# Kernel tuning notes

Hardware: AMD Instinct MI355X
Metric: run time of the kernel (lower is better)

The kernel has to match this reference:

```python
import jax, jax.numpy as jnp
import numpy as np

B, Q, S, D, H, F = 16, 8, 4096, 2048, 16, 128  # batch, new tokens, past kv, d_state, heads, head_dim
W_SCALE = 0.02  # keep projections well-conditioned for stable softmax


def setup_inputs() -> dict:
    key = jax.random.key(0)
    ks = jax.random.split(key, 8)
    return {
        "x": jax.random.normal(ks[0], (B, Q, D), jnp.float32),
        "cache_k": jax.random.normal(ks[1], (B, S, H, F), jnp.float32),
        "cache_v": jax.random.normal(ks[2], (B, S, H, F), jnp.float32),
        "wq": jax.random.normal(ks[3], (D, H, F), jnp.float32) * W_SCALE,
        "bq": jnp.zeros((H, F), jnp.float32),
        "wk": jax.random.normal(ks[4], (D, H, F), jnp.float32) * W_SCALE,
        "bk": jnp.zeros((H, F), jnp.float32),
        "wv": jax.random.normal(ks[5], (D, H, F), jnp.float32) * W_SCALE,
        "bv": jnp.zeros((H, F), jnp.float32),
        "wo": jax.random.normal(ks[6], (H, F, D), jnp.float32) * W_SCALE,
        "bo": jnp.zeros((D,), jnp.float32),
    }


def reference(x, cache_k, cache_v, wq, bq, wk, bk, wv, bv, wo, bo):
    # QKV projections: DenseGeneral(features=(H, F), axis=-1)
    q = jnp.einsum("bqd,dhf->bqhf", x, wq) + bq          # [B,Q,H,F]
    k_new = jnp.einsum("bqd,dhf->bqhf", x, wk) + bk      # [B,Q,H,F]
    v_new = jnp.einsum("bqd,dhf->bqhf", x, wv) + bv
    # concat-based KV cache growth along the sequence axis (axis=1)
    k = jnp.concatenate([cache_k, k_new], axis=1)        # [B,S+Q,H,F]
    v = jnp.concatenate([cache_v, v_new], axis=1)
    # full dot-product attention over the whole cache (mask=None on decode path)
    scale = 1.0 / jnp.sqrt(jnp.asarray(F, q.dtype))
    scores = jnp.einsum("bqhf,bkhf->bhqk", q, k) * scale  # [B,H,Q,S+Q]
    probs = jax.nn.softmax(scores, axis=-1)
    attn = jnp.einsum("bhqk,bkhf->bhqf", probs, v)        # [B,H,Q,F]
    # output projection: DenseGeneral(features=D, axis=(-3,-1)) contracts (H, F)
    out = jnp.einsum("bhqf,hfd->bqd", attn, wo) + bo      # [B,Q,D]
    return (out, k, v)
```

## Files before the change

### kernel.cpp

```cpp
#include <hip/hip_runtime.h>
#include <hip/hip_bf16.h>

constexpr int Bc = 16;
constexpr int Qc = 8;
constexpr int Sc = 4096;
constexpr int Dc = 2048;
constexpr int Hc = 16;
constexpr int Fc = 128;
constexpr int SP = Sc + Qc;
constexpr int Mr = Bc * Qc;
constexpr int CHUNK = 256;
constexpr int NCHUNK = 16;
constexpr float SCALE = 0.08838834764831845f;
constexpr float LOG2E = 1.4426950408889634f;
constexpr float QSCALE = SCALE * LOG2E;
constexpr int GKS = 8;
constexpr int GKS_O = 16;

typedef float floatx4 __attribute__((ext_vector_type(4)));

__device__ __forceinline__ float4 nt_load4(const float* p) {
    floatx4 r = __builtin_nontemporal_load(reinterpret_cast<const floatx4*>(p));
    return make_float4(r.x, r.y, r.z, r.w);
}
__device__ __forceinline__ void nt_store4(float* p, float4 v) {
    floatx4 r; r.x = v.x; r.y = v.y; r.z = v.z; r.w = v.w;
    __builtin_nontemporal_store(r, reinterpret_cast<floatx4*>(p));
}

template<int KS>
__global__ __launch_bounds__(256)
void gemm_ksplit(const float* __restrict__ A, const float* __restrict__ W0,
                 const float* __restrict__ W1, const float* __restrict__ W2,
                 float* __restrict__ part)
{
    constexpr int KC = Dc / KS;
    const int ntile = blockIdx.x;
    const int mat   = blockIdx.y;
    const int kz    = blockIdx.z;
    const float* __restrict__ W = (mat == 0) ? W0 : ((mat == 1) ? W1 : W2);
    const int t  = threadIdx.x;
    const int tx = t & 15, ty = t >> 4;
    const int r0 = ty * 8, c0 = tx * 8;
    const int ncol0 = ntile * 128;

    __shared__ float a_s[16][132];
    __shared__ float w_s[16][128];

    float acc[8][8] = {};

    const int kbase = kz * KC;
    for (int k0 = kbase; k0 < kbase + KC; k0 += 16) {
        {
            const int kk = t & 15, r = t >> 4;
            #pragma unroll
            for (int i = 0; i < 8; i++)
                a_s[kk][r + i * 16] = A[(size_t)(r + i * 16) * Dc + k0 + kk];
        }
        {
            const int nn = t & 127, ks_ = t >> 7;
            #pragma unroll
            for (int i = 0; i < 8; i++)
                w_s[ks_ + i * 2][nn] = W[(size_t)(k0 + ks_ + i * 2) * 2048 + ncol0 + nn];
        }
        __syncthreads();
        #pragma unroll
        for (int kk = 0; kk < 16; kk++) {
            const float4 av0 = *reinterpret_cast<const float4*>(&a_s[kk][r0]);
            const float4 av1 = *reinterpret_cast<const float4*>(&a_s[kk][r0 + 4]);
            const float4 wv0 = *reinterpret_cast<const float4*>(&w_s[kk][c0]);
            const float4 wv1 = *reinterpret_cast<const float4*>(&w_s[kk][c0 + 4]);
            const float av[8] = {av0.x, av0.y, av0.z, av0.w, av1.x, av1.y, av1.z, av1.w};
            const float wv[8] = {wv0.x, wv0.y, wv0.z, wv0.w, wv1.x, wv1.y, wv1.z, wv1.w};
            #pragma unroll
            for (int i = 0; i < 8; i++)
                #pragma unroll
                for (int j = 0; j < 8; j++)
                    acc[i][j] += av[i] * wv[j];
        }
        __syncthreads();
    }
    float* __restrict__ dst = part + (size_t)(mat * KS + kz) * Mr * 2048;
    #pragma unroll
    for (int i = 0; i < 8; i++)
        #pragma unroll
        for (int j = 0; j < 8; j++)
            dst[(size_t)(r0 + i) * 2048 + ncol0 + c0 + j] = acc[i][j];
}

__global__ __launch_bounds__(256)
void reduce_qkv(const float* __restrict__ part, const float* __restrict__ bq,
                const float* __restrict__ bk, const float* __restrict__ bv,
                float* __restrict__ q_ws, float* __restrict__ out_k, float* __restrict__ out_v)
{
    const int mat = blockIdx.y;
    const int e4 = blockIdx.x * 256 + threadIdx.x;
    const int e = e4 * 4;
    const int m = e >> 11, n = e & 2047;
    const float* __restrict__ p = part + (size_t)mat * GKS * (Mr * 2048);
    float4 s = make_float4(0, 0, 0, 0);
    #pragma unroll
    for (int ks = 0; ks < GKS; ks++) {
        const float4 a = *reinterpret_cast<const float4*>(&p[(size_t)ks * (Mr * 2048) + e]);
        s.x += a.x; s.y += a.y; s.z += a.z; s.w += a.w;
    }
    const int b = m >> 3, qi = m & 7;
    if (mat == 0) {
        const float4 bb = *reinterpret_cast<const float4*>(&bq[n]);
        s.x += bb.x; s.y += bb.y; s.z += bb.z; s.w += bb.w;
        *reinterpret_cast<float4*>(&q_ws[e]) = s;
    } else if (mat == 1) {
        const float4 bb = *reinterpret_cast<const float4*>(&bk[n]);
        s.x += bb.x; s.y += bb.y; s.z += bb.z; s.w += bb.w;
        *reinterpret_cast<float4*>(&out_k[((size_t)(b * SP + Sc + qi)) * 2048 + n]) = s;
    } else {
        const float4 bb = *reinterpret_cast<const float4*>(&bv[n]);
        s.x += bb.x; s.y += bb.y; s.z += bb.z; s.w += bb.w;
        *reinterpret_cast<float4*>(&out_v[((size_t)(b * SP + Sc + qi)) * 2048 + n]) = s;
    }
}

__global__ __launch_bounds__(1024, 4)
void attn_fused(const float* __restrict__ cache_k, const float* __restrict__ cache_v,
                const float* __restrict__ q_ws,
                float* __restrict__ out_k, float* __restrict__ out_v,
                float* __restrict__ part_acc, float* __restrict__ part_l)
{
    const int c = blockIdx.x;
    const int b = blockIdx.y;
    const int t = threadIdx.x;
    const int lane = t & 63;
    const int hwid = t >> 5;
    const int h = hwid & 15;
    const int par = hwid >> 4;
    const int fl = lane & 31;
    const int s0 = c * CHUNK;

    __shared__ float wacc_s[Hc][Qc][Fc];
    __shared__ float l_s[Hc][Qc];

    const int sel1 = fl & 1, sel2 = (fl >> 1) & 1, sel3 = (fl >> 2) & 1;
    const int myqi = 4 * sel1 + 2 * sel2 + sel3;
    int baddr[Qc];
    #pragma unroll
    for (int qi = 0; qi < Qc; qi++) {
        const int slot = ((qi >> 2) & 1) | (((qi >> 1) & 1) << 1) | ((qi & 1) << 2);
        baddr[qi] = (lane & ~7) | slot;
    }

    float4 qreg[Qc];
    #pragma unroll
    for (int qi = 0; qi < Qc; qi++) {
        float4 qv = *reinterpret_cast<const float4*>(
            &q_ws[((size_t)(b * Qc + qi)) * Dc + h * Fc + fl * 4]);
        qv.x *= QSCALE; qv.y *= QSCALE; qv.z *= QSCALE; qv.w *= QSCALE;
        qreg[qi] = qv;
    }

    float4 acc[Qc];
    float lsum = 0.f;
    #pragma unroll
    for (int i = 0; i < Qc; i++) acc[i] = make_float4(0, 0, 0, 0);

    const int rowoff = h * Fc + fl * 4;

    #pragma unroll 2
    for (int n = 0; n < CHUNK / 2; n++) {
        const int key = s0 + 2 * n + par;
        const size_t coff = ((size_t)(b * Sc + key)) * 2048 + rowoff;
        const size_t ooff = ((size_t)(b * SP + key)) * 2048 + rowoff;
        const float4 kv = nt_load4(&cache_k[coff]);
        const float4 vv = nt_load4(&cache_v[coff]);
        nt_store4(&out_k[ooff], kv);
        nt_store4(&out_v[ooff], vv);

        float p[Qc];
        #pragma unroll
        for (int qi = 0; qi < Qc; qi++)
            p[qi] = kv.x * qreg[qi].x + kv.y * qreg[qi].y
                  + kv.z * qreg[qi].z + kv.w * qreg[qi].w;
        float a1[4];
        #pragma unroll
        for (int i = 0; i < 4; i++) {
            const float send = sel1 ? p[i] : p[i + 4];
            const float keep = sel1 ? p[i + 4] : p[i];
            a1[i] = keep + __shfl_xor(send, 1, 64);
        }
        float a2[2];
        #pragma unroll
        for (int i = 0; i < 2; i++) {
            const float send = sel2 ? a1[i] : a1[i + 2];
            const float keep = sel2 ? a1[i + 2] : a1[i];
            a2[i] = keep + __shfl_xor(send, 2, 64);
        }
        float s_ = (sel3 ? a2[1] : a2[0]) + __shfl_xor(sel3 ? a2[0] : a2[1], 4, 64);
        s_ += __shfl_xor(s_, 8, 64);
        s_ += __shfl_xor(s_, 16, 64);
        const float e = __builtin_amdgcn_exp2f(s_);
        lsum += e;
        #pragma unroll
        for (int qi = 0; qi < Qc; qi++) {
            const float pe = __shfl(e, baddr[qi], 64);
            acc[qi].x += pe * vv.x; acc[qi].y += pe * vv.y;
            acc[qi].z += pe * vv.z; acc[qi].w += pe * vv.w;
        }
    }

    if (c == NCHUNK - 1) {
        #pragma unroll
        for (int m = 0; m < Qc / 2; m++) {
            const int key = Sc + 2 * m + par;
            const size_t ooff = ((size_t)(b * SP + key)) * 2048 + rowoff;
            const float4 kv = *reinterpret_cast<const float4*>(&out_k[ooff]);
            const float4 vv = *reinterpret_cast<const float4*>(&out_v[ooff]);

            float p[Qc];
            #pragma unroll
            for (int qi = 0; qi < Qc; qi++)
                p[qi] = kv.x * qreg[qi].x + kv.y * qreg[qi].y
                      + kv.z * qreg[qi].z + kv.w * qreg[qi].w;
            float a1[4];
            #pragma unroll
            for (int i = 0; i < 4; i++) {
                const float send = sel1 ? p[i] : p[i + 4];
                const float keep = sel1 ? p[i + 4] : p[i];
                a1[i] = keep + __shfl_xor(send, 1, 64);
            }
            float a2[2];
            #pragma unroll
            for (int i = 0; i < 2; i++) {
                const float send = sel2 ? a1[i] : a1[i + 2];
                const float keep = sel2 ? a1[i + 2] : a1[i];
                a2[i] = keep + __shfl_xor(send, 2, 64);
            }
            float s_ = (sel3 ? a2[1] : a2[0]) + __shfl_xor(sel3 ? a2[0] : a2[1], 4, 64);
            s_ += __shfl_xor(s_, 8, 64);
            s_ += __shfl_xor(s_, 16, 64);
            const float e = __builtin_amdgcn_exp2f(s_);
            lsum += e;
            #pragma unroll
            for (int qi = 0; qi < Qc; qi++) {
                const float pe = __shfl(e, baddr[qi], 64);
                acc[qi].x += pe * vv.x; acc[qi].y += pe * vv.y;
                acc[qi].z += pe * vv.z; acc[qi].w += pe * vv.w;
            }
        }
    }

    if (par == 0) {
        #pragma unroll
        for (int qi = 0; qi < Qc; qi++)
            *reinterpret_cast<float4*>(&wacc_s[h][qi][fl * 4]) = acc[qi];
        if (fl < 8) l_s[h][myqi] = lsum;
    }
    __syncthreads();
    if (par == 1) {
        const size_t idx = (size_t)(b * Hc + h) * NCHUNK + c;
        #pragma unroll
        for (int qi = 0; qi < Qc; qi++) {
            const float4 a = *reinterpret_cast<const float4*>(&wacc_s[h][qi][fl * 4]);
            float4 s_;
            s_.x = a.x + acc[qi].x; s_.y = a.y + acc[qi].y;
            s_.z = a.z + acc[qi].z; s_.w = a.w + acc[qi].w;
            *reinterpret_cast<float4*>(&part_acc[(idx * Qc + qi) * Fc + fl * 4]) = s_;
        }
        if (fl < 8) part_l[idx * Qc + myqi] = l_s[h][myqi] + lsum;
    }
}

__global__ __launch_bounds__(256)
void attn_combine(const float* __restrict__ part_acc, const float* __restrict__ part_l,
                  float* __restrict__ attn_ws)
{
    const int bh = blockIdx.x;
    const int b = bh >> 4, h = bh & 15;
    const int t = threadIdx.x;
    const int qi = t >> 5, f4 = (t & 31) * 4;
    const size_t base = (size_t)bh * NCHUNK;

    float lg = 0.f;
    #pragma unroll
    for (int c = 0; c < NCHUNK; c++) lg += part_l[(base + c) * Qc + qi];
    float4 s_ = make_float4(0, 0, 0, 0);
    #pragma unroll
    for (int c = 0; c < NCHUNK; c++) {
        const float4 a = *reinterpret_cast<const float4*>(
            &part_acc[((base + c) * Qc + qi) * Fc + f4]);
        s_.x += a.x; s_.y += a.y; s_.z += a.z; s_.w += a.w;
    }
    const float inv = 1.0f / lg;
    const float4 o = make_float4(s_.x * inv, s_.y * inv, s_.z * inv, s_.w * inv);
    *reinterpret_cast<float4*>(&attn_ws[((size_t)(b * Qc + qi)) * Dc + h * Fc + f4]) = o;
}

__global__ __launch_bounds__(256)
void reduce_o(const float* __restrict__ part, const float* __restrict__ bo,
              float* __restrict__ out)
{
    const int e4 = blockIdx.x * 256 + threadIdx.x;
    const int e = e4 * 4;
    const int n = e & 2047;
    float4 s = make_float4(0, 0, 0, 0);
    #pragma unroll
    for (int ks = 0; ks < GKS_O; ks++) {
        const float4 a = *reinterpret_cast<const float4*>(&part[(size_t)ks * (Mr * 2048) + e]);
        s.x += a.x; s.y += a.y; s.z += a.z; s.w += a.w;
    }
    const float4 bb = *reinterpret_cast<const float4*>(&bo[n]);
    s.x += bb.x; s.y += bb.y; s.z += bb.z; s.w += bb.w;
    *reinterpret_cast<float4*>(&out[e]) = s;
}

extern "C" void kernel_launch(void* const* d_in, const int* in_sizes, int n_in,
                              void* d_out, int out_size, void* d_ws, size_t ws_size,
                              hipStream_t stream)
{
    (void)in_sizes; (void)n_in; (void)out_size; (void)ws_size;
    const float* x       = (const float*)d_in[0];
    const float* cache_k = (const float*)d_in[1];
    const float* cache_v = (const float*)d_in[2];
    const float* wq      = (const float*)d_in[3];
    const float* bq      = (const float*)d_in[4];
    const float* wk      = (const float*)d_in[5];
    const float* bk      = (const float*)d_in[6];
    const float* wv      = (const float*)d_in[7];
    const float* bv      = (const float*)d_in[8];
    const float* wo      = (const float*)d_in[9];
    const float* bo      = (const float*)d_in[10];

    float* out   = (float*)d_out;
    float* out_k = out + (size_t)Mr * Dc;
    float* out_v = out_k + (size_t)Bc * SP * Hc * Fc;

    float* ws       = (float*)d_ws;
    float* q_ws     = ws;
    float* attn_ws  = ws + 262144;
    float* part_l   = ws + 524288;
    float* gemm_part = ws + 557056;
    float* part_acc = gemm_part;

    gemm_ksplit<GKS><<<dim3(16, 3, GKS), 256, 0, stream>>>(x, wq, wk, wv, gemm_part);
    reduce_qkv<<<dim3(256, 3), 256, 0, stream>>>(gemm_part, bq, bk, bv, q_ws, out_k, out_v);
    attn_fused<<<dim3(NCHUNK, Bc), 1024, 0, stream>>>(
        cache_k, cache_v, q_ws, out_k, out_v, part_acc, part_l);
    attn_combine<<<dim3(Bc * Hc), 256, 0, stream>>>(part_acc, part_l, attn_ws);
    gemm_ksplit<GKS_O><<<dim3(16, 1, GKS_O), 256, 0, stream>>>(attn_ws, wo, wo, wo, gemm_part);
    reduce_o<<<dim3(256), 256, 0, stream>>>(gemm_part, bo, out);
}
```

Before: 505.4 us.

## Split attention chunk into score pass and PV pass via shared memory

The single key loop is split into two passes. The first loads K, computes exp scores and writes them to a shared-memory buffer of CHUNK×H×Q floats. The second loads V and reads those scores back as float4s, replacing eight cross-lane shuffles per key with two LDS loads. Shared memory grows to about 128KB per block, which may limit occupancy. Each thread only reads scores its own wave wrote, since lanes with fl<8 of the same wave store them.

```diff
diff --git a/kernel.cpp b/kernel.cpp
--- a/kernel.cpp
+++ b/kernel.cpp
@@ -136,7 +136,7 @@
     const int fl = lane & 31;
     const int s0 = c * CHUNK;
 
-    __shared__ float wacc_s[Hc][Qc][Fc];
+    __shared__ float sc_s[CHUNK][Hc][Qc];
     __shared__ float l_s[Hc][Qc];
 
     const int sel1 = fl & 1, sel2 = (fl >> 1) & 1, sel3 = (fl >> 2) & 1;
@@ -166,13 +166,12 @@
 
     #pragma unroll 2
     for (int n = 0; n < CHUNK / 2; n++) {
-        const int key = s0 + 2 * n + par;
+        const int kl = 2 * n + par;
+        const int key = s0 + kl;
         const size_t coff = ((size_t)(b * Sc + key)) * 2048 + rowoff;
         const size_t ooff = ((size_t)(b * SP + key)) * 2048 + rowoff;
         const float4 kv = nt_load4(&cache_k[coff]);
-        const float4 vv = nt_load4(&cache_v[coff]);
         nt_store4(&out_k[ooff], kv);
-        nt_store4(&out_v[ooff], vv);
 
         float p[Qc];
         #pragma unroll
@@ -198,12 +197,28 @@
         s_ += __shfl_xor(s_, 16, 64);
         const float e = __builtin_amdgcn_exp2f(s_);
         lsum += e;
-        #pragma unroll
-        for (int qi = 0; qi < Qc; qi++) {
-            const float pe = __shfl(e, baddr[qi], 64);
-            acc[qi].x += pe * vv.x; acc[qi].y += pe * vv.y;
-            acc[qi].z += pe * vv.z; acc[qi].w += pe * vv.w;
-        }
+        if (fl < 8) sc_s[kl][h][myqi] = e;
+    }
+
+    #pragma unroll 2
+    for (int n = 0; n < CHUNK / 2; n++) {
+        const int kl = 2 * n + par;
+        const int key = s0 + kl;
+        const size_t coff = ((size_t)(b * Sc + key)) * 2048 + rowoff;
+        const size_t ooff = ((size_t)(b * SP + key)) * 2048 + rowoff;
+        const float4 vv = nt_load4(&cache_v[coff]);
+        nt_store4(&out_v[ooff], vv);
+
+        const float4 e0 = *reinterpret_cast<const float4*>(&sc_s[kl][h][0]);
+        const float4 e1 = *reinterpret_cast<const float4*>(&sc_s[kl][h][4]);
+        acc[0].x += e0.x * vv.x; acc[0].y += e0.x * vv.y; acc[0].z += e0.x * vv.z; acc[0].w += e0.x * vv.w;
+        acc[1].x += e0.y * vv.x; acc[1].y += e0.y * vv.y; acc[1].z += e0.y * vv.z; acc[1].w += e0.y * vv.w;
+        acc[2].x += e0.z * vv.x; acc[2].y += e0.z * vv.y; acc[2].z += e0.z * vv.z; acc[2].w += e0.z * vv.w;
+        acc[3].x += e0.w * vv.x; acc[3].y += e0.w * vv.y; acc[3].z += e0.w * vv.z; acc[3].w += e0.w * vv.w;
+        acc[4].x += e1.x * vv.x; acc[4].y += e1.x * vv.y; acc[4].z += e1.x * vv.z; acc[4].w += e1.x * vv.w;
+        acc[5].x += e1.y * vv.x; acc[5].y += e1.y * vv.y; acc[5].z += e1.y * vv.z; acc[5].w += e1.y * vv.w;
+        acc[6].x += e1.z * vv.x; acc[6].y += e1.z * vv.y; acc[6].z += e1.z * vv.z; acc[6].w += e1.z * vv.w;
+        acc[7].x += e1.w * vv.x; acc[7].y += e1.w * vv.y; acc[7].z += e1.w * vv.z; acc[7].w += e1.w * vv.w;
     }
 
     if (c == NCHUNK - 1) {
@@ -247,10 +262,12 @@
         }
     }
 
+    __syncthreads();
+    float* wacc = &sc_s[0][0][0];
     if (par == 0) {
         #pragma unroll
         for (int qi = 0; qi < Qc; qi++)
-            *reinterpret_cast<float4*>(&wacc_s[h][qi][fl * 4]) = acc[qi];
+            *reinterpret_cast<float4*>(&wacc[(h * Qc + qi) * Fc + fl * 4]) = acc[qi];
         if (fl < 8) l_s[h][myqi] = lsum;
     }
     __syncthreads();
@@ -258,7 +275,7 @@
         const size_t idx = (size_t)(b * Hc + h) * NCHUNK + c;
         #pragma unroll
         for (int qi = 0; qi < Qc; qi++) {
-            const float4 a = *reinterpret_cast<const float4*>(&wacc_s[h][qi][fl * 4]);
+            const float4 a = *reinterpret_cast<const float4*>(&wacc[(h * Qc + qi) * Fc + fl * 4]);
             float4 s_;
             s_.x = a.x + acc[qi].x; s_.y = a.y + acc[qi].y;
             s_.z = a.z + acc[qi].z; s_.w = a.w + acc[qi].w;
```

New measurement: 514.8 us. No clear change (+1.9%).

## Fuse split-K and attention reductions into producers via last-block atomic counters

Applied to the files above, without the earlier changes.

Removes the three separate reduction kernels (reduce_qkv, attn_combine, reduce_o) by having the last-arriving block of each group, detected with an atomic counter after a threadfence, perform the reduction and bias add inside the producing kernel. This cuts kernel launches and inter-kernel gaps but adds a memset for the counters. The reduction work is now done by only a few blocks per group, so it runs with less parallelism than the standalone kernels had.

```diff
diff --git a/kernel.cpp b/kernel.cpp
--- a/kernel.cpp
+++ b/kernel.cpp
@@ -28,13 +28,16 @@
     __builtin_nontemporal_store(r, reinterpret_cast<floatx4*>(p));
 }
 
-template<int KS>
 __global__ __launch_bounds__(256)
-void gemm_ksplit(const float* __restrict__ A, const float* __restrict__ W0,
-                 const float* __restrict__ W1, const float* __restrict__ W2,
-                 float* __restrict__ part)
+void gemm_qkv(const float* __restrict__ A, const float* __restrict__ W0,
+              const float* __restrict__ W1, const float* __restrict__ W2,
+              const float* __restrict__ bq, const float* __restrict__ bk,
+              const float* __restrict__ bv,
+              float* __restrict__ part, float* __restrict__ q_ws,
+              float* __restrict__ out_k, float* __restrict__ out_v,
+              int* __restrict__ cnt)
 {
-    constexpr int KC = Dc / KS;
+    constexpr int KC = Dc / GKS;
     const int ntile = blockIdx.x;
     const int mat   = blockIdx.y;
     const int kz    = blockIdx.z;
@@ -46,19 +49,18 @@
 
     __shared__ float a_s[16][132];
     __shared__ float w_s[16][128];
+    __shared__ int is_last;
 
     float acc[8][8] = {};
 
     const int kbase = kz * KC;
     for (int k0 = kbase; k0 < kbase + KC; k0 += 16) {
-        {
-            const int kk = t & 15, r = t >> 4;
+        {   const int kk = t & 15, r = t >> 4;
             #pragma unroll
             for (int i = 0; i < 8; i++)
                 a_s[kk][r + i * 16] = A[(size_t)(r + i * 16) * Dc + k0 + kk];
         }
-        {
-            const int nn = t & 127, ks_ = t >> 7;
+        {   const int nn = t & 127, ks_ = t >> 7;
             #pragma unroll
             for (int i = 0; i < 8; i++)
                 w_s[ks_ + i * 2][nn] = W[(size_t)(k0 + ks_ + i * 2) * 2048 + ncol0 + nn];
@@ -80,43 +82,42 @@
         }
         __syncthreads();
     }
-    float* __restrict__ dst = part + (size_t)(mat * KS + kz) * Mr * 2048;
+    float* __restrict__ dst = part + (size_t)(mat * GKS + kz) * Mr * 2048;
     #pragma unroll
     for (int i = 0; i < 8; i++)
         #pragma unroll
         for (int j = 0; j < 8; j++)
             dst[(size_t)(r0 + i) * 2048 + ncol0 + c0 + j] = acc[i][j];
-}
-
-__global__ __launch_bounds__(256)
-void reduce_qkv(const float* __restrict__ part, const float* __restrict__ bq,
-                const float* __restrict__ bk, const float* __restrict__ bv,
-                float* __restrict__ q_ws, float* __restrict__ out_k, float* __restrict__ out_v)
-{
-    const int mat = blockIdx.y;
-    const int e4 = blockIdx.x * 256 + threadIdx.x;
-    const int e = e4 * 4;
-    const int m = e >> 11, n = e & 2047;
-    const float* __restrict__ p = part + (size_t)mat * GKS * (Mr * 2048);
-    float4 s = make_float4(0, 0, 0, 0);
-    #pragma unroll
-    for (int ks = 0; ks < GKS; ks++) {
-        const float4 a = *reinterpret_cast<const float4*>(&p[(size_t)ks * (Mr * 2048) + e]);
-        s.x += a.x; s.y += a.y; s.z += a.z; s.w += a.w;
-    }
-    const int b = m >> 3, qi = m & 7;
-    if (mat == 0) {
-        const float4 bb = *reinterpret_cast<const float4*>(&bq[n]);
+
+    __threadfence();
+    __syncthreads();
+    if (t == 0) is_last = (atomicAdd(&cnt[mat * 16 + ntile], 1) == GKS - 1);
+    __syncthreads();
+    if (!is_last) return;
+    __threadfence();
+    const float* __restrict__ bias = (mat == 0) ? bq : ((mat == 1) ? bk : bv);
+    const float* __restrict__ pbase = part + (size_t)mat * GKS * (Mr * 2048);
+    #pragma unroll
+    for (int it = 0; it < 16; it++) {
+        const int idx = it * 256 + t;
+        const int row = idx >> 5;
+        const int n = ncol0 + (idx & 31) * 4;
+        float4 s = make_float4(0, 0, 0, 0);
+        #pragma unroll
+        for (int ks = 0; ks < GKS; ks++) {
+            const float4 a = *reinterpret_cast<const float4*>(
+                &pbase[(size_t)ks * (Mr * 2048) + (size_t)row * 2048 + n]);
+            s.x += a.x; s.y += a.y; s.z += a.z; s.w += a.w;
+        }
+        const float4 bb = *reinterpret_cast<const float4*>(&bias[n]);
         s.x += bb.x; s.y += bb.y; s.z += bb.z; s.w += bb.w;
-        *reinterpret_cast<float4*>(&q_ws[e]) = s;
-    } else if (mat == 1) {
-        const float4 bb = *reinterpret_cast<const float4*>(&bk[n]);
-        s.x += bb.x; s.y += bb.y; s.z += bb.z; s.w += bb.w;
-        *reinterpret_cast<float4*>(&out_k[((size_t)(b * SP + Sc + qi)) * 2048 + n]) = s;
-    } else {
-        const float4 bb = *reinterpret_cast<const float4*>(&bv[n]);
-        s.x += bb.x; s.y += bb.y; s.z += bb.z; s.w += bb.w;
-        *reinterpret_cast<float4*>(&out_v[((size_t)(b * SP + Sc + qi)) * 2048 + n]) = s;
+        const int b = row >> 3, qi = row & 7;
+        if (mat == 0)
+            *reinterpret_cast<float4*>(&q_ws[(size_t)row * 2048 + n]) = s;
+        else if (mat == 1)
+            *reinterpret_cast<float4*>(&out_k[((size_t)(b * SP + Sc + qi)) * 2048 + n]) = s;
+        else
+            *reinterpret_cast<float4*>(&out_v[((size_t)(b * SP + Sc + qi)) * 2048 + n]) = s;
     }
 }
 
@@ -124,7 +125,8 @@
 void attn_fused(const float* __restrict__ cache_k, const float* __restrict__ cache_v,
                 const float* __restrict__ q_ws,
                 float* __restrict__ out_k, float* __restrict__ out_v,
-                float* __restrict__ part_acc, float* __restrict__ part_l)
+                float* __restrict__ part_acc, float* __restrict__ part_l,
+                float* __restrict__ attn_ws, int* __restrict__ cnt_b)
 {
     const int c = blockIdx.x;
     const int b = blockIdx.y;
@@ -138,6 +140,7 @@
 
     __shared__ float wacc_s[Hc][Qc][Fc];
     __shared__ float l_s[Hc][Qc];
+    __shared__ int is_last;
 
     const int sel1 = fl & 1, sel2 = (fl >> 1) & 1, sel3 = (fl >> 2) & 1;
     const int myqi = 4 * sel1 + 2 * sel2 + sel3;
@@ -266,49 +269,114 @@
         }
         if (fl < 8) part_l[idx * Qc + myqi] = l_s[h][myqi] + lsum;
     }
+
+    __threadfence();
+    __syncthreads();
+    if (t == 0) is_last = (atomicAdd(&cnt_b[b], 1) == NCHUNK - 1);
+    __syncthreads();
+    if (!is_last) return;
+    __threadfence();
+    #pragma unroll
+    for (int it = 0; it < 4; it++) {
+        const int idx = it * 1024 + t;
+        const int h2 = idx >> 8;
+        const int qi = (idx >> 5) & 7;
+        const int f4v = (idx & 31) * 4;
+        const size_t base2 = (size_t)(b * Hc + h2) * NCHUNK;
+        float lg = 0.f;
+        float4 s_ = make_float4(0, 0, 0, 0);
+        #pragma unroll
+        for (int cc = 0; cc < NCHUNK; cc++) {
+            lg += part_l[(base2 + cc) * Qc + qi];
+            const float4 a = *reinterpret_cast<const float4*>(
+                &part_acc[((base2 + cc) * Qc + qi) * Fc + f4v]);
+            s_.x += a.x; s_.y += a.y; s_.z += a.z; s_.w += a.w;
+        }
+        const float inv = 1.0f / lg;
+        const float4 o = make_float4(s_.x * inv, s_.y * inv, s_.z * inv, s_.w * inv);
+        *reinterpret_cast<float4*>(
+            &attn_ws[((size_t)(b * Qc + qi)) * Dc + h2 * Fc + f4v]) = o;
+    }
 }
 
 __global__ __launch_bounds__(256)
-void attn_combine(const float* __restrict__ part_acc, const float* __restrict__ part_l,
-                  float* __restrict__ attn_ws)
+void gemm_o(const float* __restrict__ A, const float* __restrict__ W,
+            const float* __restrict__ bo,
+            float* __restrict__ part, float* __restrict__ out,
+            int* __restrict__ cnt)
 {
-    const int bh = blockIdx.x;
-    const int b = bh >> 4, h = bh & 15;
-    const int t = threadIdx.x;
-    const int qi = t >> 5, f4 = (t & 31) * 4;
-    const size_t base = (size_t)bh * NCHUNK;
-
-    float lg = 0.f;
-    #pragma unroll
-    for (int c = 0; c < NCHUNK; c++) lg += part_l[(base + c) * Qc + qi];
-    float4 s_ = make_float4(0, 0, 0, 0);
-    #pragma unroll
-    for (int c = 0; c < NCHUNK; c++) {
-        const float4 a = *reinterpret_cast<const float4*>(
-            &part_acc[((base + c) * Qc + qi) * Fc + f4]);
-        s_.x += a.x; s_.y += a.y; s_.z += a.z; s_.w += a.w;
-    }
-    const float inv = 1.0f / lg;
-    const float4 o = make_float4(s_.x * inv, s_.y * inv, s_.z * inv, s_.w * inv);
-    *reinterpret_cast<float4*>(&attn_ws[((size_t)(b * Qc + qi)) * Dc + h * Fc + f4]) = o;
-}
-
-__global__ __launch_bounds__(256)
-void reduce_o(const float* __restrict__ part, const float* __restrict__ bo,
-              float* __restrict__ out)
-{
-    const int e4 = blockIdx.x * 256 + threadIdx.x;
-    const int e = e4 * 4;
-    const int n = e & 2047;
-    float4 s = make_float4(0, 0, 0, 0);
-    #pragma unroll
-    for (int ks = 0; ks < GKS_O; ks++) {
-        const float4 a = *reinterpret_cast<const float4*>(&part[(size_t)ks * (Mr * 2048) + e]);
-        s.x += a.x; s.y += a.y; s.z += a.z; s.w += a.w;
-    }
-    const float4 bb = *reinterpret_cast<const float4*>(&bo[n]);
-    s.x += bb.x; s.y += bb.y; s.z += bb.z; s.w += bb.w;
-    *reinterpret_cast<float4*>(&out[e]) = s;
+    constexpr int KC = Dc / GKS_O;
+    const int ntile = blockIdx.x;
+    const int kz    = blockIdx.y;
+    const int t  = threadIdx.x;
+    const int tx = t & 15, ty = t >> 4;
+    const int r0 = ty * 8, c0 = tx * 8;
+    const int ncol0 = ntile * 128;
+
+    __shared__ float a_s[16][132];
+    __shared__ float w_s[16][128];
+    __shared__ int is_last;
+
+    float acc[8][8] = {};
+
+    const int kbase = kz * KC;
+    for (int k0 = kbase; k0 < kbase + KC; k0 += 16) {
+        {   const int kk = t & 15, r = t >> 4;
+            #pragma unroll
+            for (int i = 0; i < 8; i++)
+                a_s[kk][r + i * 16] = A[(size_t)(r + i * 16) * Dc + k0 + kk];
+        }
+        {   const int nn = t & 127, ks_ = t >> 7;
+            #pragma unroll
+            for (int i = 0; i < 8; i++)
+                w_s[ks_ + i * 2][nn] = W[(size_t)(k0 + ks_ + i * 2) * 2048 + ncol0 + nn];
+        }
+        __syncthreads();
+        #pragma unroll
+        for (int kk = 0; kk < 16; kk++) {
+            const float4 av0 = *reinterpret_cast<const float4*>(&a_s[kk][r0]);
+            const float4 av1 = *reinterpret_cast<const float4*>(&a_s[kk][r0 + 4]);
+            const float4 wv0 = *reinterpret_cast<const float4*>(&w_s[kk][c0]);
+            const float4 wv1 = *reinterpret_cast<const float4*>(&w_s[kk][c0 + 4]);
+            const float av[8] = {av0.x, av0.y, av0.z, av0.w, av1.x, av1.y, av1.z, av1.w};
+            const float wv[8] = {wv0.x, wv0.y, wv0.z, wv0.w, wv1.x, wv1.y, wv1.z, wv1.w};
+            #pragma unroll
+            for (int i = 0; i < 8; i++)
+                #pragma unroll
+                for (int j = 0; j < 8; j++)
+                    acc[i][j] += av[i] * wv[j];
+        }
+        __syncthreads();
+    }
+    float* __restrict__ dst = part + (size_t)kz * Mr * 2048;
+    #pragma unroll
+    for (int i = 0; i < 8; i++)
+        #pragma unroll
+        for (int j = 0; j < 8; j++)
+            dst[(size_t)(r0 + i) * 2048 + ncol0 + c0 + j] = acc[i][j];
+
+    __threadfence();
+    __syncthreads();
+    if (t == 0) is_last = (atomicAdd(&cnt[ntile], 1) == GKS_O - 1);
+    __syncthreads();
+    if (!is_last) return;
+    __threadfence();
+    #pragma unroll
+    for (int it = 0; it < 16; it++) {
+        const int idx = it * 256 + t;
+        const int row = idx >> 5;
+        const int n = ncol0 + (idx & 31) * 4;
+        float4 s = make_float4(0, 0, 0, 0);
+        #pragma unroll
+        for (int ks = 0; ks < GKS_O; ks++) {
+            const float4 a = *reinterpret_cast<const float4*>(
+                &part[(size_t)ks * (Mr * 2048) + (size_t)row * 2048 + n]);
+            s.x += a.x; s.y += a.y; s.z += a.z; s.w += a.w;
+        }
+        const float4 bb = *reinterpret_cast<const float4*>(&bo[n]);
+        s.x += bb.x; s.y += bb.y; s.z += bb.z; s.w += bb.w;
+        *reinterpret_cast<float4*>(&out[(size_t)row * 2048 + n]) = s;
+    }
 }
 
 extern "C" void kernel_launch(void* const* d_in, const int* in_sizes, int n_in,
@@ -336,14 +404,18 @@
     float* q_ws     = ws;
     float* attn_ws  = ws + 262144;
     float* part_l   = ws + 524288;
-    float* gemm_part = ws + 557056;
+    int*   cnts     = (int*)(ws + 557056);
+    float* gemm_part = ws + 557184;
     float* part_acc = gemm_part;
-
-    gemm_ksplit<GKS><<<dim3(16, 3, GKS), 256, 0, stream>>>(x, wq, wk, wv, gemm_part);
-    reduce_qkv<<<dim3(256, 3), 256, 0, stream>>>(gemm_part, bq, bk, bv, q_ws, out_k, out_v);
+    int* cnt_qkv = cnts;
+    int* cnt_b   = cnts + 48;
+    int* cnt_o   = cnts + 64;
+
+    hipMemsetAsync(cnts, 0, 512, stream);
+    gemm_qkv<<<dim3(16, 3, GKS), 256, 0, stream>>>(
+        x, wq, wk, wv, bq, bk, bv, gemm_part, q_ws, out_k, out_v, cnt_qkv);
     attn_fused<<<dim3(NCHUNK, Bc), 1024, 0, stream>>>(
-        cache_k, cache_v, q_ws, out_k, out_v, part_acc, part_l);
-    attn_combine<<<dim3(Bc * Hc), 256, 0, stream>>>(part_acc, part_l, attn_ws);
-    gemm_ksplit<GKS_O><<<dim3(16, 1, GKS_O), 256, 0, stream>>>(attn_ws, wo, wo, wo, gemm_part);
-    reduce_o<<<dim3(256), 256, 0, stream>>>(gemm_part, bo, out);
-}
+        cache_k, cache_v, q_ws, out_k, out_v, part_acc, part_l, attn_ws, cnt_b);
+    gemm_o<<<dim3(16, GKS_O), 256, 0, stream>>>(
+        attn_ws, wo, bo, gemm_part, out, cnt_o);
+}
```

Result: slower. 770.8 us (+52.5%).
